# Kernel tuning notes

Measured on AMD Instinct MI355X. Metric: run time of the kernel, lower is better.

Reference implementation:

```python
import jax, jax.numpy as jnp
import numpy as np

B, L, S, H, E, D = 4, 2048, 2048, 8, 64, 64

def setup_inputs() -> dict:
    key = jax.random.key(0)
    kq, kk, kv = jax.random.split(key, 3)
    queries = jax.random.normal(kq, (B, L, H, E), dtype=jnp.float32)
    keys = jax.random.normal(kk, (B, S, H, E), dtype=jnp.float32)
    values = jax.random.normal(kv, (B, S, H, D), dtype=jnp.float32)
    # TriangularCausalMask: True above the diagonal (positions to mask)
    causal = jnp.triu(jnp.ones((L, S), dtype=bool), k=1)
    attn_mask = jnp.broadcast_to(causal[None, None], (B, 1, L, S))
    return {"queries": queries, "keys": keys, "values": values, "attn_mask": attn_mask}

def reference(queries, keys, values, attn_mask):
    scale = 1.0 / jnp.sqrt(jnp.asarray(E, queries.dtype))
    # scores: [B,H,L,S]
    scores = jnp.einsum('blhe,bshe->bhls', queries, keys)
    neg_inf = jnp.asarray(-jnp.inf, scores.dtype)
    scores = jnp.where(attn_mask, neg_inf, scores)
    A = jax.nn.softmax(scale * scores, axis=-1)
    # dropout is identity in eval mode
    V = jnp.einsum('bhls,bshd->blhd', A, values)
    return V
```

## Files before the change

### kernel.cpp

```cpp
#include <hip/hip_runtime.h>
#include <math.h>

typedef __attribute__((ext_vector_type(8))) short bf16x8;
typedef __attribute__((ext_vector_type(4))) float f32x4;
typedef __attribute__((ext_vector_type(4))) unsigned int u32x4;

#define B_ 4
#define L_ 2048
#define S_ 2048
#define H_ 8
#define E_ 64
#define D_ 64
#define NT_ 32
#define TILE_BYTES 16384
#define WS_NEEDED ((size_t)B_ * H_ * NT_ * TILE_BYTES)
#define SCL (0.125f * 1.44269504088896f)

__device__ __forceinline__ unsigned short f2bf(float x) {
    unsigned int u = __builtin_bit_cast(unsigned int, x);
    u += 0x7fffu + ((u >> 16) & 1u);
    return (unsigned short)(u >> 16);
}
__device__ __forceinline__ int rho(int r) {
    return (r & 32) | (((r >> 2) & 1) << 4) | (((r >> 3) & 3) << 2) | (r & 3);
}
__device__ __forceinline__ void gload16(const void* g, void* l) {
    __builtin_amdgcn_global_load_lds((const __attribute__((address_space(1))) unsigned int*)g,
                                     (__attribute__((address_space(3))) unsigned int*)l, 16, 0, 0);
}

__global__ __launch_bounds__(256) void prep_kv(const float* __restrict__ K,
                                               const float* __restrict__ V,
                                               unsigned short* __restrict__ ws)
{
    __shared__ __align__(16) unsigned short vt[64][80];
    const int tid = threadIdx.x;
    const int bid = blockIdx.x;
    const int kt  = bid >> 5;
    const int bh  = (((bid >> 3) & 3) << 3) | (bid & 7);
    const int b   = bh >> 3, h = bh & 7;
    const int s0  = kt * 64;
    const int r   = tid >> 2;
    const int e0  = (tid & 3) * 16;

    const float* krow = K + (((size_t)(b * S_ + s0 + r)) * H_ + h) * E_ + e0;
    const float* vrow = V + (((size_t)(b * S_ + s0 + r)) * H_ + h) * D_ + e0;
    char* tile = (char*)(ws) + ((size_t)(bh * NT_ + kt) * TILE_BYTES);

    unsigned short kb[16];
    #pragma unroll
    for (int i = 0; i < 4; ++i) {
        f32x4 k4 = *(const f32x4*)(krow + i * 4);
        #pragma unroll
        for (int jq = 0; jq < 4; ++jq) kb[i * 4 + jq] = f2bf(k4[jq]);
    }
    {
        const int rr = rho(r);
        const int m  = (rr & 7) << 4;
        char* kbase = tile + rr * 128;
        u32x4 lo, hi;
        #pragma unroll
        for (int jq = 0; jq < 4; ++jq) {
            lo[jq] = (unsigned)kb[2 * jq] | ((unsigned)kb[2 * jq + 1] << 16);
            hi[jq] = (unsigned)kb[8 + 2 * jq] | ((unsigned)kb[9 + 2 * jq] << 16);
        }
        *(u32x4*)(kbase + ((2 * e0) ^ m))      = lo;
        *(u32x4*)(kbase + ((2 * e0 + 16) ^ m)) = hi;
    }
    #pragma unroll
    for (int i = 0; i < 4; ++i) {
        f32x4 v4 = *(const f32x4*)(vrow + i * 4);
        #pragma unroll
        for (int jq = 0; jq < 4; ++jq) vt[e0 + i * 4 + jq][r] = f2bf(v4[jq]);
    }
    __syncthreads();
    {
        const int d  = tid >> 2;
        const int c0 = (tid & 3) * 16;
        const int m  = (d & 7) << 4;
        char* vbase = tile + 8192 + d * 128;
        u32x4 lo = *(const u32x4*)&vt[d][c0];
        u32x4 hi = *(const u32x4*)&vt[d][c0 + 8];
        *(u32x4*)(vbase + ((2 * c0) ^ m))      = lo;
        *(u32x4*)(vbase + ((2 * c0 + 16) ^ m)) = hi;
    }
}

#define STAGE(I, BUF) do { \
    const char* sa = tb + (size_t)(I) * TILE_BYTES; \
    const char* sb = tb + (size_t)(jj + 1 + (I)) * TILE_BYTES; \
    char* da = pool + (BUF) * 16384 + tid * 16; \
    char* db = pool + 32768 + (BUF) * 16384 + tid * 16; \
    gload16(sa + tid * 16, da); \
    gload16(sa + 8192 + tid * 16, da + 8192); \
    gload16(sb + tid * 16, db); \
    gload16(sb + 8192 + tid * 16, db + 8192); \
} while (0)

__global__ __launch_bounds__(512, 4) void attn11(const float* __restrict__ Q,
                                                 const unsigned short* __restrict__ ws,
                                                 float* __restrict__ O)
{
    __shared__ __align__(16) char pool[65536];

    const int tid  = threadIdx.x;
    const int lane = tid & 63;
    const int w    = tid >> 6;
    const int team = w >> 2;
    const int tw   = w & 3;
    const int lq   = lane & 15;
    const int g    = lane >> 4;

    const int bid = blockIdx.x;
    const int bh  = bid & 31;
    const int q   = bid >> 5;
    const int jj  = (q < 8) ? (15 - q) : (q - 8);
    const int b0  = bh >> 3, h = bh & 7;

    const int q0 = jj * 128 + tw * 32;
    int qrow[2];
    qrow[0] = q0 + lq;
    qrow[1] = q0 + 16 + lq;
    const int dktB = 2 * jj + (tw >> 1);

    bf16x8 qf[2][2];
    #pragma unroll
    for (int qs = 0; qs < 2; ++qs) {
        const float* qptr = Q + (((size_t)(b0 * L_ + qrow[qs])) * H_ + h) * E_;
        #pragma unroll
        for (int eb = 0; eb < 2; ++eb) {
            const float* pq = qptr + eb * 32 + g * 8;
            f32x4 a = *(const f32x4*)pq;
            f32x4 b = *(const f32x4*)(pq + 4);
            bf16x8 qv;
            #pragma unroll
            for (int k = 0; k < 4; ++k) {
                qv[k]     = (short)f2bf(a[k] * SCL);
                qv[4 + k] = (short)f2bf(b[k] * SCL);
            }
            qf[qs][eb] = qv;
        }
    }

    f32x4 acc[2][4] = {};
    float ls[2] = {0.f, 0.f};

    const char* tb = (const char*)ws + (size_t)bh * NT_ * TILE_BYTES;

    STAGE(0, 0);

    int cur = 0;
    for (int i = 0; i <= jj; ++i) {
        if (i < jj) {
            STAGE(i + 1, cur ^ 1);
            asm volatile("s_waitcnt vmcnt(4)" ::: "memory");
        } else {
            asm volatile("s_waitcnt vmcnt(0)" ::: "memory");
        }
        __builtin_amdgcn_s_barrier();
        __builtin_amdgcn_sched_barrier(0);

        const int kt = team ? (jj + 1 + i) : i;
        const bool active = (team == 0) || (kt <= dktB);
        if (active) {
            const char* Kl = pool + team * 32768 + cur * 16384;
            const char* Vl = Kl + 8192;
            const int kv0 = kt * 64;
            const bool maskit = (kt >= 2 * jj);

            u32x4 pw[2][2];
            #pragma unroll
            for (int st = 0; st < 4; ++st) {
                const int row = st * 16 + lq;
                const int mm = (row & 7) << 4;
                const char* kr = Kl + row * 128;
                bf16x8 k0 = *(const bf16x8*)(kr + ((16 * g) ^ mm));
                bf16x8 k1 = *(const bf16x8*)(kr + ((64 + 16 * g) ^ mm));
                #pragma unroll
                for (int qs = 0; qs < 2; ++qs) {
                    f32x4 z = {0.f, 0.f, 0.f, 0.f};
                    __builtin_amdgcn_s_setprio(1);
                    f32x4 cc = __builtin_amdgcn_mfma_f32_16x16x32_bf16(k0, qf[qs][0], z, 0, 0, 0);
                    cc = __builtin_amdgcn_mfma_f32_16x16x32_bf16(k1, qf[qs][1], cc, 0, 0, 0);
                    __builtin_amdgcn_s_setprio(0);
                    if (maskit) {
                        #pragma unroll
                        for (int r = 0; r < 4; ++r) {
                            const int kv = kv0 + 32 * (st >> 1) + 8 * g + 4 * (st & 1) + r;
                            if (kv > qrow[qs]) cc[r] = -INFINITY;
                        }
                    }
                    f32x4 ev;
                    #pragma unroll
                    for (int r = 0; r < 4; ++r)
                        asm("v_exp_f32 %0, %1" : "=v"(ev[r]) : "v"(cc[r]));
                    ls[qs] += (ev[0] + ev[1]) + (ev[2] + ev[3]);
                    asm("v_cvt_pk_bf16_f32 %0, %1, %2" : "=v"(pw[qs][st >> 1][2 * (st & 1)])     : "v"(ev[0]), "v"(ev[1]));
                    asm("v_cvt_pk_bf16_f32 %0, %1, %2" : "=v"(pw[qs][st >> 1][2 * (st & 1) + 1]) : "v"(ev[2]), "v"(ev[3]));
                }
            }

            #pragma unroll
            for (int dt = 0; dt < 4; ++dt) {
                const int row = dt * 16 + lq;
                const int mm = (row & 7) << 4;
                bf16x8 v0 = *(const bf16x8*)(Vl + row * 128 + ((16 * g) ^ mm));
                bf16x8 v1 = *(const bf16x8*)(Vl + row * 128 + ((64 + 16 * g) ^ mm));
                __builtin_amdgcn_s_setprio(1);
                #pragma unroll
                for (int qs = 0; qs < 2; ++qs) {
                    acc[qs][dt] = __builtin_amdgcn_mfma_f32_16x16x32_bf16(v0, __builtin_bit_cast(bf16x8, pw[qs][0]), acc[qs][dt], 0, 0, 0);
                    acc[qs][dt] = __builtin_amdgcn_mfma_f32_16x16x32_bf16(v1, __builtin_bit_cast(bf16x8, pw[qs][1]), acc[qs][dt], 0, 0, 0);
                }
                __builtin_amdgcn_s_setprio(0);
            }
        }

        __builtin_amdgcn_s_barrier();
        cur ^= 1;
    }

    __builtin_amdgcn_s_barrier();
    float* sacc = (float*)pool;
    float* sls  = (float*)(pool + 128 * 68 * 4);
    if (team == 1) {
        #pragma unroll
        for (int qs = 0; qs < 2; ++qs) {
            const int rowl = 32 * tw + 16 * qs + lq;
            float l = ls[qs] + __shfl_xor(ls[qs], 16);
            l += __shfl_xor(l, 32);
            if (g == 0) sls[rowl] = l;
            #pragma unroll
            for (int dt = 0; dt < 4; ++dt)
                *(f32x4*)&sacc[rowl * 68 + dt * 16 + 4 * g] = acc[qs][dt];
        }
    }
    __syncthreads();
    if (team == 0) {
        #pragma unroll
        for (int qs = 0; qs < 2; ++qs) {
            const int rowl = 32 * tw + 16 * qs + lq;
            float l = ls[qs] + __shfl_xor(ls[qs], 16);
            l += __shfl_xor(l, 32);
            const float inv = 1.0f / (l + sls[rowl]);
            float* op = O + (((size_t)(b0 * L_ + qrow[qs])) * H_ + h) * D_;
            #pragma unroll
            for (int dt = 0; dt < 4; ++dt) {
                f32x4 p = *(const f32x4*)&sacc[rowl * 68 + dt * 16 + 4 * g];
                f32x4 o;
                #pragma unroll
                for (int r = 0; r < 4; ++r) o[r] = (acc[qs][dt][r] + p[r]) * inv;
                *(f32x4*)(op + dt * 16 + 4 * g) = o;
            }
        }
    }
}

#define KPITCH 72
__global__ __launch_bounds__(256, 2) void attn_fwd_fb(
    const float* __restrict__ Q, const float* __restrict__ K,
    const float* __restrict__ V, float* __restrict__ O)
{
    __shared__ unsigned short Klds[64 * KPITCH];
    __shared__ unsigned short Vlds[64 * KPITCH];
    const int tid = threadIdx.x, lane = tid & 63, w = tid >> 6;
    const int lq = lane & 15, g = lane >> 4;
    const int bid = blockIdx.x, qb = bid & 31, bh = bid >> 5;
    const int b0 = bh >> 3, h = bh & 7;
    const int q0 = qb * 64, qrow = q0 + w * 16 + lq;
    const float* qptr = Q + ((size_t)(b0 * L_ + qrow) * H_ + h) * E_;
    bf16x8 qf[2];
    #pragma unroll
    for (int eb = 0; eb < 2; ++eb) {
        const float* pp = qptr + eb * 32 + g * 8;
        f32x4 a = *(const f32x4*)pp; f32x4 b = *(const f32x4*)(pp + 4);
        bf16x8 qv;
        #pragma unroll
        for (int jq = 0; jq < 4; ++jq) { qv[jq] = (short)f2bf(a[jq] * 0.125f); qv[4 + jq] = (short)f2bf(b[jq] * 0.125f); }
        qf[eb] = qv;
    }
    const int tr = tid >> 2, tc = tid & 3;
    const int rh = rho(tr);
    f32x4 acc[4] = {};
    float mrow = -INFINITY, lrow = 0.f;
    for (int kt = 0; kt < qb + 1; ++kt) {
        const int kv0 = kt * 64;
        __syncthreads();
        {
            const float* krow = K + ((size_t)((b0 * S_ + kv0 + tr)) * H_ + h) * E_;
            const float* vrow = V + ((size_t)((b0 * S_ + kv0 + tr)) * H_ + h) * D_;
            #pragma unroll
            for (int i = 0; i < 4; ++i) {
                const int e0 = tc * 4 + i * 16;
                f32x4 k4 = *(const f32x4*)(krow + e0);
                unsigned int lo = (unsigned)f2bf(k4[0]) | ((unsigned)f2bf(k4[1]) << 16);
                unsigned int hi = (unsigned)f2bf(k4[2]) | ((unsigned)f2bf(k4[3]) << 16);
                *(uint2*)&Klds[rh * KPITCH + e0] = make_uint2(lo, hi);
                f32x4 v4 = *(const f32x4*)(vrow + e0);
                #pragma unroll
                for (int k2 = 0; k2 < 4; ++k2) Vlds[(e0 + k2) * KPITCH + tr] = f2bf(v4[k2]);
            }
        }
        __syncthreads();
        f32x4 sc[4];
        #pragma unroll
        for (int st = 0; st < 4; ++st) {
            const unsigned short* kr = &Klds[(st * 16 + lq) * KPITCH];
            bf16x8 ka0 = *(const bf16x8*)(kr + 8 * g);
            bf16x8 ka1 = *(const bf16x8*)(kr + 32 + 8 * g);
            f32x4 cc = {0.f, 0.f, 0.f, 0.f};
            cc = __builtin_amdgcn_mfma_f32_16x16x32_bf16(ka0, qf[0], cc, 0, 0, 0);
            cc = __builtin_amdgcn_mfma_f32_16x16x32_bf16(ka1, qf[1], cc, 0, 0, 0);
            sc[st] = cc;
        }
        float tmax = -INFINITY;
        #pragma unroll
        for (int st = 0; st < 4; ++st) {
            const int kvb = kv0 + 32 * (st >> 1) + 8 * g + 4 * (st & 1);
            #pragma unroll
            for (int r = 0; r < 4; ++r) { if (kvb + r > qrow) sc[st][r] = -INFINITY; tmax = fmaxf(tmax, sc[st][r]); }
        }
        tmax = fmaxf(tmax, __shfl_xor(tmax, 16));
        tmax = fmaxf(tmax, __shfl_xor(tmax, 32));
        const float mnew = fmaxf(mrow, tmax);
        const float corr = __expf(mrow - mnew);
        float pv[4][4]; float tsum = 0.f;
        #pragma unroll
        for (int st = 0; st < 4; ++st)
            #pragma unroll
            for (int r = 0; r < 4; ++r) { float e = __expf(sc[st][r] - mnew); pv[st][r] = e; tsum += e; }
        tsum += __shfl_xor(tsum, 16); tsum += __shfl_xor(tsum, 32);
        lrow = lrow * corr + tsum; mrow = mnew;
        #pragma unroll
        for (int dt = 0; dt < 4; ++dt)
            #pragma unroll
            for (int r = 0; r < 4; ++r) acc[dt][r] *= corr;
        bf16x8 pb[2];
        #pragma unroll
        for (int bb = 0; bb < 2; ++bb)
            #pragma unroll
            for (int s = 0; s < 2; ++s)
                #pragma unroll
                for (int r = 0; r < 4; ++r) pb[bb][4 * s + r] = (short)f2bf(pv[2 * bb + s][r]);
        #pragma unroll
        for (int bb = 0; bb < 2; ++bb)
            #pragma unroll
            for (int dt = 0; dt < 4; ++dt) {
                bf16x8 va = *(const bf16x8*)&Vlds[(dt * 16 + lq) * KPITCH + 32 * bb + 8 * g];
                acc[dt] = __builtin_amdgcn_mfma_f32_16x16x32_bf16(va, pb[bb], acc[dt], 0, 0, 0);
            }
    }
    const float inv = 1.0f / lrow;
    float* optr = O + ((size_t)(b0 * L_ + qrow) * H_ + h) * D_;
    #pragma unroll
    for (int dt = 0; dt < 4; ++dt) {
        f32x4 o;
        #pragma unroll
        for (int r = 0; r < 4; ++r) o[r] = acc[dt][r] * inv;
        *(f32x4*)(optr + dt * 16 + 4 * g) = o;
    }
}

extern "C" void kernel_launch(void* const* d_in, const int* in_sizes, int n_in,
                              void* d_out, int out_size, void* d_ws, size_t ws_size,
                              hipStream_t stream) {
    const float* Q = (const float*)d_in[0];
    const float* K = (const float*)d_in[1];
    const float* V = (const float*)d_in[2];
    float* O = (float*)d_out;
    if (ws_size >= WS_NEEDED) {
        prep_kv<<<dim3(B_ * H_ * NT_), 256, 0, stream>>>(K, V, (unsigned short*)d_ws);
        attn11<<<dim3(512), 512, 0, stream>>>(Q, (const unsigned short*)d_ws, O);
    } else {
        attn_fwd_fb<<<dim3(B_ * H_ * 32), 256, 0, stream>>>(Q, K, V, O);
    }
}
```

Before: 41.92 us.

## Restructure attention into 256-thread blocks processing paired 64-row query groups

```diff
diff --git a/kernel.cpp b/kernel.cpp
--- a/kernel.cpp
+++ b/kernel.cpp
@@ -86,42 +86,17 @@
     }
 }
 
-#define STAGE(I, BUF) do { \
-    const char* sa = tb + (size_t)(I) * TILE_BYTES; \
-    const char* sb = tb + (size_t)(jj + 1 + (I)) * TILE_BYTES; \
-    char* da = pool + (BUF) * 16384 + tid * 16; \
-    char* db = pool + 32768 + (BUF) * 16384 + tid * 16; \
-    gload16(sa + tid * 16, da); \
-    gload16(sa + 8192 + tid * 16, da + 8192); \
-    gload16(sb + tid * 16, db); \
-    gload16(sb + 8192 + tid * 16, db + 8192); \
-} while (0)
-
-__global__ __launch_bounds__(512, 4) void attn11(const float* __restrict__ Q,
-                                                 const unsigned short* __restrict__ ws,
-                                                 float* __restrict__ O)
+__device__ __forceinline__ void do_group(
+    const float* __restrict__ Q, const char* __restrict__ tb, char* __restrict__ pool,
+    int b0, int h, int g, int team, int tw, int lq, int gl, int tid,
+    float* __restrict__ O)
 {
-    __shared__ __align__(16) char pool[65536];
-
-    const int tid  = threadIdx.x;
-    const int lane = tid & 63;
-    const int w    = tid >> 6;
-    const int team = w >> 2;
-    const int tw   = w & 3;
-    const int lq   = lane & 15;
-    const int g    = lane >> 4;
-
-    const int bid = blockIdx.x;
-    const int bh  = bid & 31;
-    const int q   = bid >> 5;
-    const int jj  = (q < 8) ? (15 - q) : (q - 8);
-    const int b0  = bh >> 3, h = bh & 7;
-
-    const int q0 = jj * 128 + tw * 32;
+    const int nt = g + 1;
+    const int nh = (nt + 1) >> 1;
+    const int q0 = g * 64 + tw * 32;
     int qrow[2];
     qrow[0] = q0 + lq;
     qrow[1] = q0 + 16 + lq;
-    const int dktB = 2 * jj + (tw >> 1);
 
     bf16x8 qf[2][2];
     #pragma unroll
@@ -129,7 +104,7 @@
         const float* qptr = Q + (((size_t)(b0 * L_ + qrow[qs])) * H_ + h) * E_;
         #pragma unroll
         for (int eb = 0; eb < 2; ++eb) {
-            const float* pq = qptr + eb * 32 + g * 8;
+            const float* pq = qptr + eb * 32 + gl * 8;
             f32x4 a = *(const f32x4*)pq;
             f32x4 b = *(const f32x4*)(pq + 4);
             bf16x8 qv;
@@ -145,28 +120,38 @@
     f32x4 acc[2][4] = {};
     float ls[2] = {0.f, 0.f};
 
-    const char* tb = (const char*)ws + (size_t)bh * NT_ * TILE_BYTES;
-
-    STAGE(0, 0);
-
+    #define STAGE13(I, BUF) do { \
+        int tbi = nh + (I); if (tbi > nt - 1) tbi = nt - 1; \
+        const char* ga = tb + (size_t)(I) * TILE_BYTES; \
+        const char* gb = tb + (size_t)tbi * TILE_BYTES; \
+        char* la = pool + (BUF) * 16384; \
+        char* lb = pool + 32768 + (BUF) * 16384; \
+        _Pragma("unroll") \
+        for (int r4 = 0; r4 < 4; ++r4) { \
+            gload16(ga + r4 * 4096 + tid * 16, la + r4 * 4096 + tid * 16); \
+            gload16(gb + r4 * 4096 + tid * 16, lb + r4 * 4096 + tid * 16); \
+        } \
+    } while (0)
+
+    STAGE13(0, 0);
     int cur = 0;
-    for (int i = 0; i <= jj; ++i) {
-        if (i < jj) {
-            STAGE(i + 1, cur ^ 1);
-            asm volatile("s_waitcnt vmcnt(4)" ::: "memory");
+    for (int i = 0; i < nh; ++i) {
+        if (i + 1 < nh) {
+            STAGE13(i + 1, cur ^ 1);
+            asm volatile("s_waitcnt vmcnt(8)" ::: "memory");
         } else {
             asm volatile("s_waitcnt vmcnt(0)" ::: "memory");
         }
         __builtin_amdgcn_s_barrier();
         __builtin_amdgcn_sched_barrier(0);
 
-        const int kt = team ? (jj + 1 + i) : i;
-        const bool active = (team == 0) || (kt <= dktB);
+        const int kt = team ? (nh + i) : i;
+        const bool active = team ? (kt < nt) : true;
         if (active) {
             const char* Kl = pool + team * 32768 + cur * 16384;
             const char* Vl = Kl + 8192;
             const int kv0 = kt * 64;
-            const bool maskit = (kt >= 2 * jj);
+            const bool maskit = (kt == g);
 
             u32x4 pw[2][2];
             #pragma unroll
@@ -174,8 +159,8 @@
                 const int row = st * 16 + lq;
                 const int mm = (row & 7) << 4;
                 const char* kr = Kl + row * 128;
-                bf16x8 k0 = *(const bf16x8*)(kr + ((16 * g) ^ mm));
-                bf16x8 k1 = *(const bf16x8*)(kr + ((64 + 16 * g) ^ mm));
+                bf16x8 k0 = *(const bf16x8*)(kr + ((16 * gl) ^ mm));
+                bf16x8 k1 = *(const bf16x8*)(kr + ((64 + 16 * gl) ^ mm));
                 #pragma unroll
                 for (int qs = 0; qs < 2; ++qs) {
                     f32x4 z = {0.f, 0.f, 0.f, 0.f};
@@ -186,7 +171,7 @@
                     if (maskit) {
                         #pragma unroll
                         for (int r = 0; r < 4; ++r) {
-                            const int kv = kv0 + 32 * (st >> 1) + 8 * g + 4 * (st & 1) + r;
+                            const int kv = kv0 + 32 * (st >> 1) + 8 * gl + 4 * (st & 1) + r;
                             if (kv > qrow[qs]) cc[r] = -INFINITY;
                         }
                     }
@@ -204,8 +189,8 @@
             for (int dt = 0; dt < 4; ++dt) {
                 const int row = dt * 16 + lq;
                 const int mm = (row & 7) << 4;
-                bf16x8 v0 = *(const bf16x8*)(Vl + row * 128 + ((16 * g) ^ mm));
-                bf16x8 v1 = *(const bf16x8*)(Vl + row * 128 + ((64 + 16 * g) ^ mm));
+                bf16x8 v0 = *(const bf16x8*)(Vl + row * 128 + ((16 * gl) ^ mm));
+                bf16x8 v1 = *(const bf16x8*)(Vl + row * 128 + ((64 + 16 * gl) ^ mm));
                 __builtin_amdgcn_s_setprio(1);
                 #pragma unroll
                 for (int qs = 0; qs < 2; ++qs) {
@@ -215,45 +200,70 @@
                 __builtin_amdgcn_s_setprio(0);
             }
         }
-
         __builtin_amdgcn_s_barrier();
         cur ^= 1;
     }
-
-    __builtin_amdgcn_s_barrier();
+    #undef STAGE13
+
     float* sacc = (float*)pool;
-    float* sls  = (float*)(pool + 128 * 68 * 4);
+    float* sls  = (float*)(pool + 64 * 68 * 4);
     if (team == 1) {
         #pragma unroll
         for (int qs = 0; qs < 2; ++qs) {
-            const int rowl = 32 * tw + 16 * qs + lq;
+            const int rowl = tw * 32 + qs * 16 + lq;
             float l = ls[qs] + __shfl_xor(ls[qs], 16);
             l += __shfl_xor(l, 32);
-            if (g == 0) sls[rowl] = l;
+            if (gl == 0) sls[rowl] = l;
             #pragma unroll
             for (int dt = 0; dt < 4; ++dt)
-                *(f32x4*)&sacc[rowl * 68 + dt * 16 + 4 * g] = acc[qs][dt];
+                *(f32x4*)&sacc[rowl * 68 + dt * 16 + 4 * gl] = acc[qs][dt];
         }
     }
     __syncthreads();
     if (team == 0) {
         #pragma unroll
         for (int qs = 0; qs < 2; ++qs) {
-            const int rowl = 32 * tw + 16 * qs + lq;
+            const int rowl = tw * 32 + qs * 16 + lq;
             float l = ls[qs] + __shfl_xor(ls[qs], 16);
             l += __shfl_xor(l, 32);
             const float inv = 1.0f / (l + sls[rowl]);
             float* op = O + (((size_t)(b0 * L_ + qrow[qs])) * H_ + h) * D_;
             #pragma unroll
             for (int dt = 0; dt < 4; ++dt) {
-                f32x4 p = *(const f32x4*)&sacc[rowl * 68 + dt * 16 + 4 * g];
+                f32x4 p = *(const f32x4*)&sacc[rowl * 68 + dt * 16 + 4 * gl];
                 f32x4 o;
                 #pragma unroll
                 for (int r = 0; r < 4; ++r) o[r] = (acc[qs][dt][r] + p[r]) * inv;
-                *(f32x4*)(op + dt * 16 + 4 * g) = o;
-            }
-        }
-    }
+                *(f32x4*)(op + dt * 16 + 4 * gl) = o;
+            }
+        }
+    }
+    __syncthreads();
+}
+
+__global__ __launch_bounds__(256, 2) void attn13(const float* __restrict__ Q,
+                                                 const unsigned short* __restrict__ ws,
+                                                 float* __restrict__ O)
+{
+    __shared__ __align__(16) char pool[65536];
+
+    const int tid  = threadIdx.x;
+    const int lane = tid & 63;
+    const int w    = tid >> 6;
+    const int team = w >> 1;
+    const int tw   = w & 1;
+    const int lq   = lane & 15;
+    const int gl   = lane >> 4;
+
+    const int bid = blockIdx.x;
+    const int bh  = bid & 31;
+    const int pr  = bid >> 5;
+    const int b0  = bh >> 3, h = bh & 7;
+
+    const char* tb = (const char*)ws + (size_t)bh * NT_ * TILE_BYTES;
+
+    do_group(Q, tb, pool, b0, h, pr,      team, tw, lq, gl, tid, O);
+    do_group(Q, tb, pool, b0, h, 31 - pr, team, tw, lq, gl, tid, O);
 }
 
 #define KPITCH 72
@@ -370,7 +380,7 @@
     float* O = (float*)d_out;
     if (ws_size >= WS_NEEDED) {
         prep_kv<<<dim3(B_ * H_ * NT_), 256, 0, stream>>>(K, V, (unsigned short*)d_ws);
-        attn11<<<dim3(512), 512, 0, stream>>>(Q, (const unsigned short*)d_ws, O);
+        attn13<<<dim3(512), 256, 0, stream>>>(Q, (const unsigned short*)d_ws, O);
     } else {
         attn_fwd_fb<<<dim3(B_ * H_ * 32), 256, 0, stream>>>(Q, K, V, O);
     }
```

Result: slower. 43.94 us (+4.8%).
